# Optimization experiments

Hardware: AMD Instinct MI355X
Metric: run time of the kernel (lower is better)

The kernel has to match this reference:

```python
import jax, jax.numpy as jnp
import numpy as np

SEQ_LEN = 512
EMBED_DIM = 768
MAX_SPAN_LEN = 16
WIDTH_EMB_DIM = 50
NUM_SPAN_LABELS = 9
N_SPANS = 32768


def setup_inputs() -> dict:
    key = jax.random.key(0)
    ks = jax.random.split(key, 6)
    sequence_output = jax.random.normal(ks[0], (1, SEQ_LEN, EMBED_DIM), dtype=jnp.float32)
    # start in [0, SEQ_LEN - MAX_SPAN_LEN) so end = start + width stays a valid index
    start_indices = jax.random.randint(ks[1], (N_SPANS,), 0, SEQ_LEN - MAX_SPAN_LEN)
    span_widths = jax.random.randint(ks[2], (N_SPANS,), 1, MAX_SPAN_LEN + 1)  # width >= 1 (mean over non-empty slice)
    end_indices = start_indices + span_widths
    width_table = jax.random.normal(ks[3], (MAX_SPAN_LEN + 1, WIDTH_EMB_DIM), dtype=jnp.float32) * 0.02
    W = jax.random.normal(ks[4], (NUM_SPAN_LABELS, 3 * EMBED_DIM + WIDTH_EMB_DIM), dtype=jnp.float32) * 0.02
    b = jnp.zeros((NUM_SPAN_LABELS,), dtype=jnp.float32)
    return {
        "sequence_output": sequence_output,
        "start_indices": start_indices,
        "end_indices": end_indices,
        "span_widths": span_widths,
        "width_table": width_table,
        "W": W,
        "b": b,
    }


def reference(sequence_output, start_indices, end_indices, span_widths, width_table, W, b):
    # sequence_output: [1, S, D]; batch is asserted to be 1 in the original module.
    seq = sequence_output[0]                       # [S, D]
    h_start = seq[start_indices]                   # [N, D] gather of start tokens
    h_end = seq[end_indices]                       # [N, D] gather of end tokens
    # Ragged mean over seq[s:e] (exclusive end), vectorized via exclusive prefix sums:
    # mean = (cumsum[e] - cumsum[s]) / (e - s)
    cs = jnp.concatenate([jnp.zeros((1, seq.shape[-1]), seq.dtype), jnp.cumsum(seq, axis=0)], axis=0)  # [S+1, D]
    widths_f = span_widths[:, None].astype(seq.dtype)
    h_span_avg = (cs[end_indices] - cs[start_indices]) / widths_f   # [N, D]
    width_emb = width_table[span_widths]            # [N, 50]
    span_rep = jnp.concatenate([h_start, h_end, h_span_avg, width_emb], axis=-1)  # [N, 3D+50]
    logits = span_rep @ W.T + b                     # [N, num_labels]
    return logits
```

## Files before the change

### kernel.cpp

```cpp
#include <hip/hip_runtime.h>

#define SEQ_LEN 512
#define EMBED_DIM 768
#define WIDTH_EMB 50
#define NUM_LABELS 9
#define N_SPANS 32768
#define WROW (3 * EMBED_DIM + WIDTH_EMB)

#define P1_OFF 0
#define P2_OFF (SEQ_LEN * NUM_LABELS)
#define P3_OFF (2 * SEQ_LEN * NUM_LABELS)
#define WP_OFF (3 * SEQ_LEN * NUM_LABELS)

__global__ __launch_bounds__(64) void proj_kernel(
    const float* __restrict__ seq,
    const float* __restrict__ wtab,
    const float* __restrict__ W,
    const float* __restrict__ b,
    float* __restrict__ ws)
{
    const int blk  = blockIdx.x;
    const int lane = threadIdx.x;

    if (blk < SEQ_LEN) {
        const float* srow = seq + blk * EMBED_DIM;
        float s[12];
#pragma unroll
        for (int k = 0; k < 12; ++k) s[k] = srow[lane + 64 * k];

#pragma unroll
        for (int seg = 0; seg < 3; ++seg) {
#pragma unroll
            for (int l = 0; l < NUM_LABELS; ++l) {
                const float* wrow = W + l * WROW + seg * EMBED_DIM;
                float p = 0.f;
#pragma unroll
                for (int k = 0; k < 12; ++k) p += s[k] * wrow[lane + 64 * k];
#pragma unroll
                for (int off = 32; off > 0; off >>= 1)
                    p += __shfl_xor(p, off, 64);
                if (lane == 0)
                    ws[seg * (SEQ_LEN * NUM_LABELS) + blk * NUM_LABELS + l] = p;
            }
        }
    } else {
        for (int idx = lane; idx < 17 * NUM_LABELS; idx += 64) {
            int w = idx / NUM_LABELS;
            int l = idx - w * NUM_LABELS;
            const float* wrow = W + l * WROW + 3 * EMBED_DIM;
            const float* trow = wtab + w * WIDTH_EMB;
            float p = b[l];
            for (int j = 0; j < WIDTH_EMB; ++j) p += trow[j] * wrow[j];
            ws[WP_OFF + idx] = p;
        }
    }
}

__global__ __launch_bounds__(256) void span_kernel(
    const int* __restrict__ start_idx,
    const int* __restrict__ end_idx,
    const int* __restrict__ widths,
    const float* __restrict__ ws,
    float* __restrict__ out)
{
    const int i = blockIdx.x * blockDim.x + threadIdx.x;
    if (i >= N_SPANS * NUM_LABELS) return;
    const int n = i / NUM_LABELS;
    const int l = i - n * NUM_LABELS;

    const int s = start_idx[n];
    const int e = end_idx[n];
    const int w = widths[n];

    const float* P1 = ws + P1_OFF;
    const float* P2 = ws + P2_OFF;
    const float* P3 = ws + P3_OFF;
    const float* WP = ws + WP_OFF;

    float acc = P1[s * NUM_LABELS + l] + P2[e * NUM_LABELS + l]
              + WP[w * NUM_LABELS + l];
    float sum = 0.f;
    for (int t = s; t < e; ++t) sum += P3[t * NUM_LABELS + l];
    out[i] = acc + sum / (float)w;
}

extern "C" void kernel_launch(void* const* d_in, const int* in_sizes, int n_in,
                              void* d_out, int out_size, void* d_ws, size_t ws_size,
                              hipStream_t stream) {
    const float* seq  = (const float*)d_in[0];
    const int*   s    = (const int*)d_in[1];
    const int*   e    = (const int*)d_in[2];
    const int*   w    = (const int*)d_in[3];
    const float* wtab = (const float*)d_in[4];
    const float* W    = (const float*)d_in[5];
    const float* b    = (const float*)d_in[6];
    float* out = (float*)d_out;
    float* ws  = (float*)d_ws;

    proj_kernel<<<SEQ_LEN + 1, 64, 0, stream>>>(seq, wtab, W, b, ws);

    const int total = N_SPANS * NUM_LABELS;
    span_kernel<<<(total + 255) / 256, 256, 0, stream>>>(s, e, w, ws, out);
}
```

Baseline: 83.65 us.

## Stage P3 and width projections in LDS per block, vectorize proj loads

The span kernel now launches 576-thread blocks covering 64 spans and first copies the full P3 projection table (512x9) and the width-projection table into shared memory, so the ragged-sum loop reads LDS instead of global/L2. The projection kernel switches to float2 loads of the sequence row and weight rows to halve the load instruction count. The trade-off is that every block re-loads about 18KB of P3 from global memory plus a barrier, and the larger LDS footprint limits occupancy.

```diff
diff --git a/kernel.cpp b/kernel.cpp
--- a/kernel.cpp
+++ b/kernel.cpp
@@ -23,19 +23,23 @@
     const int lane = threadIdx.x;
 
     if (blk < SEQ_LEN) {
-        const float* srow = seq + blk * EMBED_DIM;
-        float s[12];
+        const float2* srow = (const float2*)(seq + blk * EMBED_DIM);
+        float2 s2[6];
 #pragma unroll
-        for (int k = 0; k < 12; ++k) s[k] = srow[lane + 64 * k];
+        for (int k = 0; k < 6; ++k) s2[k] = srow[lane + 64 * k];
 
 #pragma unroll
         for (int seg = 0; seg < 3; ++seg) {
 #pragma unroll
             for (int l = 0; l < NUM_LABELS; ++l) {
-                const float* wrow = W + l * WROW + seg * EMBED_DIM;
+                const float2* wrow =
+                    (const float2*)(W + l * WROW + seg * EMBED_DIM);
                 float p = 0.f;
 #pragma unroll
-                for (int k = 0; k < 12; ++k) p += s[k] * wrow[lane + 64 * k];
+                for (int k = 0; k < 6; ++k) {
+                    float2 wv = wrow[lane + 64 * k];
+                    p += s2[k].x * wv.x + s2[k].y * wv.y;
+                }
 #pragma unroll
                 for (int off = 32; off > 0; off >>= 1)
                     p += __shfl_xor(p, off, 64);
@@ -56,32 +60,37 @@
     }
 }
 
-__global__ __launch_bounds__(256) void span_kernel(
+#define SPB 64
+__global__ __launch_bounds__(576) void span_kernel(
     const int* __restrict__ start_idx,
     const int* __restrict__ end_idx,
     const int* __restrict__ widths,
     const float* __restrict__ ws,
     float* __restrict__ out)
 {
-    const int i = blockIdx.x * blockDim.x + threadIdx.x;
-    if (i >= N_SPANS * NUM_LABELS) return;
-    const int n = i / NUM_LABELS;
-    const int l = i - n * NUM_LABELS;
+    __shared__ float sP3[SEQ_LEN * NUM_LABELS];
+    __shared__ float sWP[17 * NUM_LABELS];
+
+    const int t = threadIdx.x;
+    for (int i = t; i < SEQ_LEN * NUM_LABELS; i += 576)
+        sP3[i] = ws[P3_OFF + i];
+    if (t < 17 * NUM_LABELS)
+        sWP[t] = ws[WP_OFF + t];
+    __syncthreads();
+
+    const int n = blockIdx.x * SPB + t / NUM_LABELS;
+    const int l = t - (t / NUM_LABELS) * NUM_LABELS;
 
     const int s = start_idx[n];
     const int e = end_idx[n];
     const int w = widths[n];
 
-    const float* P1 = ws + P1_OFF;
-    const float* P2 = ws + P2_OFF;
-    const float* P3 = ws + P3_OFF;
-    const float* WP = ws + WP_OFF;
-
-    float acc = P1[s * NUM_LABELS + l] + P2[e * NUM_LABELS + l]
-              + WP[w * NUM_LABELS + l];
+    float acc = ws[P1_OFF + s * NUM_LABELS + l]
+              + ws[P2_OFF + e * NUM_LABELS + l]
+              + sWP[w * NUM_LABELS + l];
     float sum = 0.f;
-    for (int t = s; t < e; ++t) sum += P3[t * NUM_LABELS + l];
-    out[i] = acc + sum / (float)w;
+    for (int k = s; k < e; ++k) sum += sP3[k * NUM_LABELS + l];
+    out[blockIdx.x * (SPB * NUM_LABELS) + t] = acc + sum / (float)w;
 }
 
 extern "C" void kernel_launch(void* const* d_in, const int* in_sizes, int n_in,
@@ -99,6 +108,5 @@
 
     proj_kernel<<<SEQ_LEN + 1, 64, 0, stream>>>(seq, wtab, W, b, ws);
 
-    const int total = N_SPANS * NUM_LABELS;
-    span_kernel<<<(total + 255) / 256, 256, 0, stream>>>(s, e, w, ws, out);
+    span_kernel<<<N_SPANS / SPB, 576, 0, stream>>>(s, e, w, ws, out);
 }
```

Measured after the change: 83.08 us. Within noise of the previous version (-0.7%).
